# Performance work log

Hardware: AMD Instinct MI355X
Metric: run time of the kernel (lower is better)

## Reference

```python
import jax, jax.numpy as jnp
import numpy as np

NUM_HEADING_BIN = 12
NUM_SIZE_CLUSTER = 8
BS = 524288
# KITTI-style mean box sizes (l, w, h) for 8 size clusters
G_MEAN_SIZE_ARR = np.array([
    [3.88, 1.63, 1.53], [0.84, 0.66, 1.76], [1.76, 0.60, 1.74], [16.17, 2.58, 3.23],
    [3.90, 1.60, 1.56], [1.73, 0.58, 1.37], [0.91, 0.48, 1.78], [2.06, 1.86, 1.66]],
    dtype=np.float32)


def setup_inputs() -> dict:
    key = jax.random.key(0)
    ks = jax.random.split(key, 13)
    f = lambda k, s: jax.random.normal(k, s, dtype=jnp.float32)
    return {
        "center": f(ks[0], (BS, 3)),
        "center_label": f(ks[1], (BS, 3)),
        "stage1_center": f(ks[2], (BS, 3)),
        "heading_scores": f(ks[3], (BS, 12)),
        "heading_residuals_normalized": f(ks[4], (BS, 12)),
        "heading_residuals": f(ks[5], (BS, 12)),
        "heading_class_label": jax.random.randint(ks[6], (BS,), 0, 12, dtype=jnp.int64),
        "heading_residuals_label": f(ks[7], (BS,)),
        "size_scores": f(ks[8], (BS, 8)),
        "size_residuals_normalized": f(ks[9], (BS, 8, 3)),
        "size_residuals": f(ks[10], (BS, 8, 3)),
        "size_class_label": jax.random.randint(ks[11], (BS,), 0, 8, dtype=jnp.int64),
        "size_residuals_label": f(ks[12], (BS, 3)),
    }


def _huber(err, delta):
    a = jnp.abs(err)
    q = jnp.minimum(a, delta)
    return jnp.mean(0.5 * q * q + delta * (a - q))


_SX = jnp.array([1, 1, -1, -1, 1, 1, -1, -1], dtype=jnp.float32)
_SY = jnp.array([1, 1, 1, 1, -1, -1, -1, -1], dtype=jnp.float32)
_SZ = jnp.array([1, -1, -1, 1, 1, -1, -1, 1], dtype=jnp.float32)


def _corners3d(centers, headings, sizes):
    # centers (bs,3), headings (bs,), sizes (bs,3) [l,w,h] -> (bs,8,3)
    l, w, h = sizes[:, 0:1], sizes[:, 1:2], sizes[:, 2:3]
    x = 0.5 * l * _SX  # (bs,8)
    y = 0.5 * h * _SY
    z = 0.5 * w * _SZ
    c = jnp.cos(headings)[:, None]
    s = jnp.sin(headings)[:, None]
    xr = c * x + s * z   # rotation about y-axis
    zr = -s * x + c * z
    return jnp.stack([xr, y, zr], axis=-1) + centers[:, None, :]


def reference(center, center_label, stage1_center, heading_scores,
              heading_residuals_normalized, heading_residuals, heading_class_label,
              heading_residuals_label, size_scores, size_residuals_normalized,
              size_residuals, size_class_label, size_residuals_label):
    corner_loss_weight, box_loss_weight = 10.0, 1.0
    mean_sizes = jnp.asarray(G_MEAN_SIZE_ARR)  # (8,3)
    hcls = heading_class_label.astype(jnp.int32)
    scls = size_class_label.astype(jnp.int32)

    center_loss = _huber(jnp.linalg.norm(center - center_label, axis=1), 2.0)
    stage1_center_loss = _huber(jnp.linalg.norm(center - stage1_center, axis=1), 1.0)

    h_logp = jax.nn.log_softmax(heading_scores, axis=1)
    heading_class_loss = -jnp.mean(jnp.take_along_axis(h_logp, hcls[:, None], axis=1))
    s_logp = jax.nn.log_softmax(size_scores, axis=1)
    size_class_loss = -jnp.mean(jnp.take_along_axis(s_logp, scls[:, None], axis=1))

    # heading residual loss (one-hot sum == gather at class index)
    hres_label_norm = heading_residuals_label / (np.pi / NUM_HEADING_BIN)
    hres_pred = jnp.take_along_axis(heading_residuals_normalized, hcls[:, None], axis=1)[:, 0]
    heading_res_loss = _huber(hres_pred - hres_label_norm, 1.0)

    # size residual loss
    sres_pred = jnp.take_along_axis(size_residuals_normalized, scls[:, None, None], axis=1)[:, 0]  # (bs,3)
    mean_size_label = mean_sizes[scls]  # (bs,3)
    sres_label_norm = size_residuals_label / mean_size_label
    size_res_loss = _huber(jnp.linalg.norm(sres_label_norm - sres_pred, axis=1), 1.0)

    # corner loss: gt_mask one-hot sum over (NH,NS) grid == gather (hcls, scls) box
    bin_centers = jnp.arange(NUM_HEADING_BIN, dtype=jnp.float32) * (2.0 * np.pi / NUM_HEADING_BIN)
    heading_pred = jnp.take_along_axis(heading_residuals, hcls[:, None], axis=1)[:, 0] + bin_centers[hcls]
    size_pred = mean_size_label + jnp.take_along_axis(size_residuals, scls[:, None, None], axis=1)[:, 0]
    corners_pred = _corners3d(center, heading_pred, size_pred)  # (bs,8,3)

    heading_label = heading_residuals_label + bin_centers[hcls]
    size_label = mean_size_label + size_residuals_label
    corners_gt = _corners3d(center_label, heading_label, size_label)
    corners_gt_flip = _corners3d(center_label, heading_label + np.pi, size_label)
    corners_dist = jnp.minimum(jnp.linalg.norm(corners_pred - corners_gt, axis=-1),
                               jnp.linalg.norm(corners_pred - corners_gt_flip, axis=-1))
    corners_loss = _huber(corners_dist, 1.0)

    total_loss = box_loss_weight * (center_loss + heading_class_loss + size_class_loss
                                    + heading_res_loss * 20.0 + size_res_loss * 20.0
                                    + stage1_center_loss + corner_loss_weight * corners_loss)
    return total_loss
```

## Files before the change

### kernel.cpp

```cpp
#include <hip/hip_runtime.h>
#include <math.h>


constexpr int BS_N = 524288;
constexpr int NBLK = 1024;

__constant__ float G_MEAN[8][3] = {
    {3.88f, 1.63f, 1.53f}, {0.84f, 0.66f, 1.76f}, {1.76f, 0.60f, 1.74f},
    {16.17f, 2.58f, 3.23f}, {3.90f, 1.60f, 1.56f}, {1.73f, 0.58f, 1.37f},
    {0.91f, 0.48f, 1.78f}, {2.06f, 1.86f, 1.66f}
};
__constant__ float G_RCP[8][3] = {
    {1.0f/3.88f, 1.0f/1.63f, 1.0f/1.53f}, {1.0f/0.84f, 1.0f/0.66f, 1.0f/1.76f},
    {1.0f/1.76f, 1.0f/0.60f, 1.0f/1.74f}, {1.0f/16.17f, 1.0f/2.58f, 1.0f/3.23f},
    {1.0f/3.90f, 1.0f/1.60f, 1.0f/1.56f}, {1.0f/1.73f, 1.0f/0.58f, 1.0f/1.37f},
    {1.0f/0.91f, 1.0f/0.48f, 1.0f/1.78f}, {1.0f/2.06f, 1.0f/1.86f, 1.0f/1.66f}
};

__device__ __forceinline__ float huber_pos(float a, float delta) {
    return (a <= delta) ? 0.5f * a * a : delta * (a - 0.5f * delta);
}
__device__ __forceinline__ float huber_norm2(float d2, float delta) {
    return (d2 <= delta * delta) ? 0.5f * d2
                                 : delta * (sqrtf(d2) - 0.5f * delta);
}
__device__ __forceinline__ float sel4(float4 v, int k) {
    float r = v.x;
    r = (k == 1) ? v.y : r;
    r = (k == 2) ? v.z : r;
    r = (k == 3) ? v.w : r;
    return r;
}
__device__ __forceinline__ float sel12(float4 a, float4 b, float4 c, int k) {
    float r = sel4(a, k);
    r = (k >= 4) ? sel4(b, k - 4) : r;
    r = (k >= 8) ? sel4(c, k - 8) : r;
    return r;
}
__device__ __forceinline__ float sel8(float4 a, float4 b, int k) {
    float r = sel4(a, k);
    r = (k >= 4) ? sel4(b, k - 4) : r;
    return r;
}

__device__ __forceinline__ float sample_loss(
    int h, int s,
    float cx, float cy, float cz,
    float lx, float ly, float lz,
    float tx, float ty, float tz,
    float4 hsA, float4 hsB, float4 hsC,
    float4 ssA, float4 ssB,
    float hrl,
    float hrnv, float hrev,
    float sl0, float sl1, float sl2,
    float sn0, float sn1, float sn2,
    float sr0, float sr1, float sr2)
{
    float contrib = 0.0f;

    const float dx0 = cx - lx, dy0 = cy - ly, dz0 = cz - lz;
    contrib += huber_norm2(dx0*dx0 + dy0*dy0 + dz0*dz0, 2.0f);
    {
        const float ax = cx - tx, ay = cy - ty, az = cz - tz;
        contrib += huber_norm2(ax*ax + ay*ay + az*az, 1.0f);
    }

    {
        float m = fmaxf(fmaxf(fmaxf(hsA.x,hsA.y),fmaxf(hsA.z,hsA.w)),
                  fmaxf(fmaxf(fmaxf(hsB.x,hsB.y),fmaxf(hsB.z,hsB.w)),
                        fmaxf(fmaxf(hsC.x,hsC.y),fmaxf(hsC.z,hsC.w))));
        float se = __expf(hsA.x-m)+__expf(hsA.y-m)+__expf(hsA.z-m)+__expf(hsA.w-m)
                 + __expf(hsB.x-m)+__expf(hsB.y-m)+__expf(hsB.z-m)+__expf(hsB.w-m)
                 + __expf(hsC.x-m)+__expf(hsC.y-m)+__expf(hsC.z-m)+__expf(hsC.w-m);
        contrib += m + __logf(se) - sel12(hsA, hsB, hsC, h);
    }
    {
        float m = fmaxf(fmaxf(fmaxf(ssA.x,ssA.y),fmaxf(ssA.z,ssA.w)),
                        fmaxf(fmaxf(ssB.x,ssB.y),fmaxf(ssB.z,ssB.w)));
        float se = __expf(ssA.x-m)+__expf(ssA.y-m)+__expf(ssA.z-m)+__expf(ssA.w-m)
                 + __expf(ssB.x-m)+__expf(ssB.y-m)+__expf(ssB.z-m)+__expf(ssB.w-m);
        contrib += m + __logf(se) - sel8(ssA, ssB, s);
    }

    contrib += 20.0f * huber_pos(fabsf(hrnv - hrl * (float)(12.0 / M_PI)), 1.0f);

    const float m0 = G_MEAN[s][0], m1 = G_MEAN[s][1], m2c = G_MEAN[s][2];
    {
        const float e0 = sl0 * G_RCP[s][0] - sn0;
        const float e1 = sl1 * G_RCP[s][1] - sn1;
        const float e2 = sl2 * G_RCP[s][2] - sn2;
        contrib += 20.0f * huber_norm2(e0*e0 + e1*e1 + e2*e2, 1.0f);
    }

    {
        const float binc = (float)h * (float)(M_PI / 6.0);
        const float hp = hrev + binc;
        const float hg = hrl + binc;
        const float lp2 = 0.5f * (m0 + sr0);
        const float wp2 = 0.5f * (m1 + sr1);
        const float hp2 = 0.5f * (m2c + sr2);
        const float lg2 = 0.5f * (m0 + sl0);
        const float wg2 = 0.5f * (m1 + sl1);
        const float hg2 = 0.5f * (m2c + sl2);
        float cp, sp, cg, sg;
        __sincosf(hp, &sp, &cp);
        __sincosf(hg, &sg, &cg);
        const float dyh = hp2 - hg2;

        constexpr float SX[8] = {1,1,-1,-1,1,1,-1,-1};
        constexpr float SY[8] = {1,1,1,1,-1,-1,-1,-1};
        constexpr float SZ[8] = {1,-1,-1,1,1,-1,-1,1};
        float csum = 0.0f;
        #pragma unroll
        for (int j = 0; j < 8; ++j) {
            const float axp = SX[j]*lp2, azp = SZ[j]*wp2;
            const float xrp = cp*axp + sp*azp;
            const float zrp = cp*azp - sp*axp;
            const float axg = SX[j]*lg2, azg = SZ[j]*wg2;
            const float xrg = cg*axg + sg*azg;
            const float zrg = cg*azg - sg*axg;
            const float ddy = dy0 + SY[j]*dyh;
            const float u = dx0 + xrp, v = dz0 + zrp;
            const float du1 = u - xrg, dv1 = v - zrg;
            const float du2 = u + xrg, dv2 = v + zrg;
            const float y2 = ddy*ddy;
            const float dgt = du1*du1 + y2 + dv1*dv1;
            const float dfl = du2*du2 + y2 + dv2*dv2;
            const float mm = fminf(dgt, dfl);
            csum += (mm <= 1.0f) ? 0.5f*mm : sqrtf(mm) - 0.5f;
        }
        contrib += 1.25f * csum;
    }
    return contrib;
}

__global__ __launch_bounds__(256) void bbox_partial(
    const float* __restrict__ center,
    const float* __restrict__ center_label,
    const float* __restrict__ stage1_center,
    const float* __restrict__ heading_scores,
    const float* __restrict__ hrn,
    const float* __restrict__ hres,
    const int*   __restrict__ hcls_in,
    const float* __restrict__ hres_label,
    const float* __restrict__ size_scores,
    const float* __restrict__ srn,
    const float* __restrict__ sres,
    const int*   __restrict__ scls_in,
    const float* __restrict__ sres_label,
    float* __restrict__ block_out)
{
    const int t  = blockIdx.x * 256 + threadIdx.x;
    const int i0 = 2 * t;

    const int2 h2 = *reinterpret_cast<const int2*>(hcls_in + i0);
    const int2 s2 = *reinterpret_cast<const int2*>(scls_in + i0);

    const float2* cp2 = reinterpret_cast<const float2*>(center        + 3*i0);
    const float2* lp2 = reinterpret_cast<const float2*>(center_label  + 3*i0);
    const float2* tp2 = reinterpret_cast<const float2*>(stage1_center + 3*i0);
    const float2* rp2 = reinterpret_cast<const float2*>(sres_label    + 3*i0);
    const float2 cA = cp2[0], cB = cp2[1], cC = cp2[2];
    const float2 lA = lp2[0], lB = lp2[1], lC = lp2[2];
    const float2 tA = tp2[0], tB = tp2[1], tC = tp2[2];
    const float2 rA = rp2[0], rB = rp2[1], rC = rp2[2];
    const float2 hl = *reinterpret_cast<const float2*>(hres_label + i0);

    const float4* hsp = reinterpret_cast<const float4*>(heading_scores + 12*i0);
    const float4 hsA0 = hsp[0], hsB0 = hsp[1], hsC0 = hsp[2];
    const float4 hsA1 = hsp[3], hsB1 = hsp[4], hsC1 = hsp[5];
    const float4* ssp = reinterpret_cast<const float4*>(size_scores + 8*i0);
    const float4 ssA0 = ssp[0], ssB0 = ssp[1];
    const float4 ssA1 = ssp[2], ssB1 = ssp[3];

    const int h0 = h2.x, h1 = h2.y, s0 = s2.x, s1 = s2.y;
    const float hrn0 = hrn [12*i0 + h0],      hrn1 = hrn [12*i0 + 12 + h1];
    const float hre0 = hres[12*i0 + h0],      hre1 = hres[12*i0 + 12 + h1];
    const int sb0 = (8*i0 + s0) * 3,          sb1 = (8*i0 + 8 + s1) * 3;
    const float sn00 = srn [sb0+0], sn01 = srn [sb0+1], sn02 = srn [sb0+2];
    const float sn10 = srn [sb1+0], sn11 = srn [sb1+1], sn12 = srn [sb1+2];
    const float sr00 = sres[sb0+0], sr01 = sres[sb0+1], sr02 = sres[sb0+2];
    const float sr10 = sres[sb1+0], sr11 = sres[sb1+1], sr12 = sres[sb1+2];

    float contrib =
        sample_loss(h0, s0,
                    cA.x, cA.y, cB.x,  lA.x, lA.y, lB.x,  tA.x, tA.y, tB.x,
                    hsA0, hsB0, hsC0,  ssA0, ssB0,
                    hl.x, hrn0, hre0,
                    rA.x, rA.y, rB.x,
                    sn00, sn01, sn02,  sr00, sr01, sr02)
      + sample_loss(h1, s1,
                    cB.y, cC.x, cC.y,  lB.y, lC.x, lC.y,  tB.y, tC.x, tC.y,
                    hsA1, hsB1, hsC1,  ssA1, ssB1,
                    hl.y, hrn1, hre1,
                    rB.y, rC.x, rC.y,
                    sn10, sn11, sn12,  sr10, sr11, sr12);

    #pragma unroll
    for (int off = 32; off > 0; off >>= 1)
        contrib += __shfl_down(contrib, off, 64);

    __shared__ float sdata[4];
    const int lane = threadIdx.x & 63;
    const int wid  = threadIdx.x >> 6;
    if (lane == 0) sdata[wid] = contrib;
    __syncthreads();
    if (threadIdx.x == 0)
        block_out[blockIdx.x] = (sdata[0] + sdata[1]) + (sdata[2] + sdata[3]);
}

__global__ __launch_bounds__(256) void bbox_final(
    const float* __restrict__ block_in, float* __restrict__ out)
{
    float ssum = 0.0f;
    for (int i = threadIdx.x; i < NBLK; i += 256)
        ssum += block_in[i];
    #pragma unroll
    for (int off = 32; off > 0; off >>= 1)
        ssum += __shfl_down(ssum, off, 64);

    __shared__ float sdata[4];
    const int lane = threadIdx.x & 63;
    const int wid  = threadIdx.x >> 6;
    if (lane == 0) sdata[wid] = ssum;
    __syncthreads();
    if (threadIdx.x == 0)
        out[0] = ((sdata[0] + sdata[1]) + (sdata[2] + sdata[3])) * (1.0f / (float)BS_N);
}

extern "C" void kernel_launch(void* const* d_in, const int* in_sizes, int n_in,
                              void* d_out, int out_size, void* d_ws, size_t ws_size,
                              hipStream_t stream) {
    const float* center        = (const float*)d_in[0];
    const float* center_label  = (const float*)d_in[1];
    const float* stage1_center = (const float*)d_in[2];
    const float* heading_sc    = (const float*)d_in[3];
    const float* hrn           = (const float*)d_in[4];
    const float* hres          = (const float*)d_in[5];
    const int*   hcls          = (const int*)d_in[6];
    const float* hres_label    = (const float*)d_in[7];
    const float* size_sc       = (const float*)d_in[8];
    const float* srn           = (const float*)d_in[9];
    const float* sres          = (const float*)d_in[10];
    const int*   scls          = (const int*)d_in[11];
    const float* sres_label    = (const float*)d_in[12];

    float* ws  = (float*)d_ws;
    float* out = (float*)d_out;

    bbox_partial<<<NBLK, 256, 0, stream>>>(
        center, center_label, stage1_center, heading_sc, hrn, hres,
        hcls, hres_label, size_sc, srn, sres, scls, sres_label, ws);
    bbox_final<<<1, 256, 0, stream>>>(ws, out);
}
```

Baseline: 41.14 us.

## Process one sample per thread and load residual rows fully as float4

Each thread now handles one sample instead of two, with 128-thread blocks and four times as many blocks. The per-class residual arrays (hrn, hres, srn, sres) are read as whole rows with float4 loads, and the needed class is picked in registers with select chains instead of data-dependent scalar gathers. This aims for more parallelism and coalesced, vectorized loads. In exchange it makes the kernel read full rows instead of a few gathered elements and uses more registers per thread.

```diff
diff --git a/kernel.cpp b/kernel.cpp
--- a/kernel.cpp
+++ b/kernel.cpp
@@ -3,7 +3,7 @@
 
 
 constexpr int BS_N = 524288;
-constexpr int NBLK = 1024;
+constexpr int NBLK = 4096;
 
 __constant__ float G_MEAN[8][3] = {
     {3.88f, 1.63f, 1.53f}, {0.84f, 0.66f, 1.76f}, {1.76f, 0.60f, 1.74f},
@@ -42,20 +42,66 @@
     r = (k >= 4) ? sel4(b, k - 4) : r;
     return r;
 }
-
-__device__ __forceinline__ float sample_loss(
-    int h, int s,
-    float cx, float cy, float cz,
-    float lx, float ly, float lz,
-    float tx, float ty, float tz,
-    float4 hsA, float4 hsB, float4 hsC,
-    float4 ssA, float4 ssB,
-    float hrl,
-    float hrnv, float hrev,
-    float sl0, float sl1, float sl2,
-    float sn0, float sn1, float sn2,
-    float sr0, float sr1, float sr2)
+__device__ __forceinline__ void sel_row3(
+    float4 a, float4 b, float4 c, float4 d, float4 e, float4 f, int s,
+    float &o0, float &o1, float &o2)
 {
+    const float r[24] = {a.x,a.y,a.z,a.w, b.x,b.y,b.z,b.w, c.x,c.y,c.z,c.w,
+                         d.x,d.y,d.z,d.w, e.x,e.y,e.z,e.w, f.x,f.y,f.z,f.w};
+    o0 = r[0]; o1 = r[1]; o2 = r[2];
+    #pragma unroll
+    for (int k = 1; k < 8; ++k) {
+        const bool m = (s == k);
+        o0 = m ? r[3*k+0] : o0;
+        o1 = m ? r[3*k+1] : o1;
+        o2 = m ? r[3*k+2] : o2;
+    }
+}
+
+__global__ __launch_bounds__(128) void bbox_partial(
+    const float* __restrict__ center,
+    const float* __restrict__ center_label,
+    const float* __restrict__ stage1_center,
+    const float* __restrict__ heading_scores,
+    const float* __restrict__ hrn,
+    const float* __restrict__ hres,
+    const int*   __restrict__ hcls_in,
+    const float* __restrict__ hres_label,
+    const float* __restrict__ size_scores,
+    const float* __restrict__ srn,
+    const float* __restrict__ sres,
+    const int*   __restrict__ scls_in,
+    const float* __restrict__ sres_label,
+    float* __restrict__ block_out)
+{
+    const int i = blockIdx.x * 128 + threadIdx.x;
+
+    const int h = hcls_in[i];
+    const int s = scls_in[i];
+
+    const float cx = center[3*i+0], cy = center[3*i+1], cz = center[3*i+2];
+    const float lx = center_label[3*i+0], ly = center_label[3*i+1], lz = center_label[3*i+2];
+    const float tx = stage1_center[3*i+0], ty = stage1_center[3*i+1], tz = stage1_center[3*i+2];
+    const float sl0 = sres_label[3*i+0], sl1 = sres_label[3*i+1], sl2 = sres_label[3*i+2];
+    const float hrl = hres_label[i];
+
+    const float4* hsp = reinterpret_cast<const float4*>(heading_scores + 12*i);
+    const float4 hsA = hsp[0], hsB = hsp[1], hsC = hsp[2];
+    const float4* ssp = reinterpret_cast<const float4*>(size_scores + 8*i);
+    const float4 ssA = ssp[0], ssB = ssp[1];
+
+    const float4* hnp = reinterpret_cast<const float4*>(hrn + 12*i);
+    const float4 hn0 = hnp[0], hn1 = hnp[1], hn2 = hnp[2];
+    const float4* hep = reinterpret_cast<const float4*>(hres + 12*i);
+    const float4 he0 = hep[0], he1 = hep[1], he2 = hep[2];
+
+    const float4* snp = reinterpret_cast<const float4*>(srn + 24*i);
+    const float4 sn0 = snp[0], sn1 = snp[1], sn2 = snp[2],
+                 sn3 = snp[3], sn4 = snp[4], sn5 = snp[5];
+    const float4* srp = reinterpret_cast<const float4*>(sres + 24*i);
+    const float4 sr0 = srp[0], sr1 = srp[1], sr2 = srp[2],
+                 sr3 = srp[3], sr4 = srp[4], sr5 = srp[5];
+
     float contrib = 0.0f;
 
     const float dx0 = cx - lx, dy0 = cy - ly, dz0 = cz - lz;
@@ -82,13 +128,19 @@
         contrib += m + __logf(se) - sel8(ssA, ssB, s);
     }
 
+    const float hrnv = sel12(hn0, hn1, hn2, h);
+    const float hrev = sel12(he0, he1, he2, h);
+    float snv0, snv1, snv2, srv0, srv1, srv2;
+    sel_row3(sn0, sn1, sn2, sn3, sn4, sn5, s, snv0, snv1, snv2);
+    sel_row3(sr0, sr1, sr2, sr3, sr4, sr5, s, srv0, srv1, srv2);
+
     contrib += 20.0f * huber_pos(fabsf(hrnv - hrl * (float)(12.0 / M_PI)), 1.0f);
 
     const float m0 = G_MEAN[s][0], m1 = G_MEAN[s][1], m2c = G_MEAN[s][2];
     {
-        const float e0 = sl0 * G_RCP[s][0] - sn0;
-        const float e1 = sl1 * G_RCP[s][1] - sn1;
-        const float e2 = sl2 * G_RCP[s][2] - sn2;
+        const float e0 = sl0 * G_RCP[s][0] - snv0;
+        const float e1 = sl1 * G_RCP[s][1] - snv1;
+        const float e2 = sl2 * G_RCP[s][2] - snv2;
         contrib += 20.0f * huber_norm2(e0*e0 + e1*e1 + e2*e2, 1.0f);
     }
 
@@ -96,9 +148,9 @@
         const float binc = (float)h * (float)(M_PI / 6.0);
         const float hp = hrev + binc;
         const float hg = hrl + binc;
-        const float lp2 = 0.5f * (m0 + sr0);
-        const float wp2 = 0.5f * (m1 + sr1);
-        const float hp2 = 0.5f * (m2c + sr2);
+        const float lp2 = 0.5f * (m0 + srv0);
+        const float wp2 = 0.5f * (m1 + srv1);
+        const float hp2 = 0.5f * (m2c + srv2);
         const float lg2 = 0.5f * (m0 + sl0);
         const float wg2 = 0.5f * (m1 + sl1);
         const float hg2 = 0.5f * (m2c + sl2);
@@ -131,82 +183,18 @@
         }
         contrib += 1.25f * csum;
     }
-    return contrib;
-}
-
-__global__ __launch_bounds__(256) void bbox_partial(
-    const float* __restrict__ center,
-    const float* __restrict__ center_label,
-    const float* __restrict__ stage1_center,
-    const float* __restrict__ heading_scores,
-    const float* __restrict__ hrn,
-    const float* __restrict__ hres,
-    const int*   __restrict__ hcls_in,
-    const float* __restrict__ hres_label,
-    const float* __restrict__ size_scores,
-    const float* __restrict__ srn,
-    const float* __restrict__ sres,
-    const int*   __restrict__ scls_in,
-    const float* __restrict__ sres_label,
-    float* __restrict__ block_out)
-{
-    const int t  = blockIdx.x * 256 + threadIdx.x;
-    const int i0 = 2 * t;
-
-    const int2 h2 = *reinterpret_cast<const int2*>(hcls_in + i0);
-    const int2 s2 = *reinterpret_cast<const int2*>(scls_in + i0);
-
-    const float2* cp2 = reinterpret_cast<const float2*>(center        + 3*i0);
-    const float2* lp2 = reinterpret_cast<const float2*>(center_label  + 3*i0);
-    const float2* tp2 = reinterpret_cast<const float2*>(stage1_center + 3*i0);
-    const float2* rp2 = reinterpret_cast<const float2*>(sres_label    + 3*i0);
-    const float2 cA = cp2[0], cB = cp2[1], cC = cp2[2];
-    const float2 lA = lp2[0], lB = lp2[1], lC = lp2[2];
-    const float2 tA = tp2[0], tB = tp2[1], tC = tp2[2];
-    const float2 rA = rp2[0], rB = rp2[1], rC = rp2[2];
-    const float2 hl = *reinterpret_cast<const float2*>(hres_label + i0);
-
-    const float4* hsp = reinterpret_cast<const float4*>(heading_scores + 12*i0);
-    const float4 hsA0 = hsp[0], hsB0 = hsp[1], hsC0 = hsp[2];
-    const float4 hsA1 = hsp[3], hsB1 = hsp[4], hsC1 = hsp[5];
-    const float4* ssp = reinterpret_cast<const float4*>(size_scores + 8*i0);
-    const float4 ssA0 = ssp[0], ssB0 = ssp[1];
-    const float4 ssA1 = ssp[2], ssB1 = ssp[3];
-
-    const int h0 = h2.x, h1 = h2.y, s0 = s2.x, s1 = s2.y;
-    const float hrn0 = hrn [12*i0 + h0],      hrn1 = hrn [12*i0 + 12 + h1];
-    const float hre0 = hres[12*i0 + h0],      hre1 = hres[12*i0 + 12 + h1];
-    const int sb0 = (8*i0 + s0) * 3,          sb1 = (8*i0 + 8 + s1) * 3;
-    const float sn00 = srn [sb0+0], sn01 = srn [sb0+1], sn02 = srn [sb0+2];
-    const float sn10 = srn [sb1+0], sn11 = srn [sb1+1], sn12 = srn [sb1+2];
-    const float sr00 = sres[sb0+0], sr01 = sres[sb0+1], sr02 = sres[sb0+2];
-    const float sr10 = sres[sb1+0], sr11 = sres[sb1+1], sr12 = sres[sb1+2];
-
-    float contrib =
-        sample_loss(h0, s0,
-                    cA.x, cA.y, cB.x,  lA.x, lA.y, lB.x,  tA.x, tA.y, tB.x,
-                    hsA0, hsB0, hsC0,  ssA0, ssB0,
-                    hl.x, hrn0, hre0,
-                    rA.x, rA.y, rB.x,
-                    sn00, sn01, sn02,  sr00, sr01, sr02)
-      + sample_loss(h1, s1,
-                    cB.y, cC.x, cC.y,  lB.y, lC.x, lC.y,  tB.y, tC.x, tC.y,
-                    hsA1, hsB1, hsC1,  ssA1, ssB1,
-                    hl.y, hrn1, hre1,
-                    rB.y, rC.x, rC.y,
-                    sn10, sn11, sn12,  sr10, sr11, sr12);
 
     #pragma unroll
     for (int off = 32; off > 0; off >>= 1)
         contrib += __shfl_down(contrib, off, 64);
 
-    __shared__ float sdata[4];
+    __shared__ float sdata[2];
     const int lane = threadIdx.x & 63;
     const int wid  = threadIdx.x >> 6;
     if (lane == 0) sdata[wid] = contrib;
     __syncthreads();
     if (threadIdx.x == 0)
-        block_out[blockIdx.x] = (sdata[0] + sdata[1]) + (sdata[2] + sdata[3]);
+        block_out[blockIdx.x] = sdata[0] + sdata[1];
 }
 
 __global__ __launch_bounds__(256) void bbox_final(
@@ -248,7 +236,7 @@
     float* ws  = (float*)d_ws;
     float* out = (float*)d_out;
 
-    bbox_partial<<<NBLK, 256, 0, stream>>>(
+    bbox_partial<<<NBLK, 128, 0, stream>>>(
         center, center_label, stage1_center, heading_sc, hrn, hres,
         hcls, hres_label, size_sc, srn, sres, scls, sres_label, ws);
     bbox_final<<<1, 256, 0, stream>>>(ws, out);
```

After: 42.57 us. +3.5%, slower.
